# Performance work log

Hardware: AMD Instinct MI355X
Metric: run time of the kernel (lower is better)

Reference implementation:

```python
import jax, jax.numpy as jnp
import numpy as np

N_NODES = 30000
N_EDGES = 480000
IN_FEATS = 256
N_HEADS = 8
OUT_FEATS = 32
EDGE_FEATS = 64
NUM_ETYPES = 8
NEG_SLOPE = 0.2


def setup_inputs() -> dict:
    key = jax.random.key(0)
    ks = jax.random.split(key, 14)
    s = 0.05
    return {
        "feat": jax.random.normal(ks[0], (N_NODES, IN_FEATS), dtype=jnp.float32),
        "e_feat": jax.random.randint(ks[1], (N_EDGES,), 0, NUM_ETYPES, dtype=jnp.int32),
        "src": jax.random.randint(ks[2], (N_EDGES,), 0, N_NODES, dtype=jnp.int32),
        "dst": jax.random.randint(ks[3], (N_EDGES,), 0, N_NODES, dtype=jnp.int32),
        # learned params (torch nn.Linear stores weight as [out, in])
        "fc_W": jax.random.normal(ks[4], (N_HEADS * OUT_FEATS, IN_FEATS), dtype=jnp.float32) * s,
        "edge_emb": jax.random.normal(ks[5], (NUM_ETYPES, EDGE_FEATS), dtype=jnp.float32) * s,
        "w_r": jnp.ones((NUM_ETYPES, 1), dtype=jnp.float32),  # init constant 1.0
        "W1": jax.random.normal(ks[6], (EDGE_FEATS * 2, EDGE_FEATS), dtype=jnp.float32) * s,
        "b1": jnp.zeros((EDGE_FEATS * 2,), dtype=jnp.float32),
        "W2": jax.random.normal(ks[7], (EDGE_FEATS * N_HEADS, EDGE_FEATS * 2), dtype=jnp.float32) * s,
        "b2": jnp.zeros((EDGE_FEATS * N_HEADS,), dtype=jnp.float32),
        "attn_l": jax.random.normal(ks[8], (1, N_HEADS, OUT_FEATS), dtype=jnp.float32) * s,
        "attn_r": jax.random.normal(ks[9], (1, N_HEADS, OUT_FEATS), dtype=jnp.float32) * s,
        "attn_e": jax.random.normal(ks[10], (1, N_HEADS, EDGE_FEATS), dtype=jnp.float32) * s,
    }


def reference(feat, e_feat, src, dst, fc_W, edge_emb, w_r, W1, b1, W2, b2,
              attn_l, attn_r, attn_e):
    # node projection: [N, H, D]
    feat_src = (feat @ fc_W.T).reshape(N_NODES, N_HEADS, OUT_FEATS)

    # edge-type embedding -> MLP -> [E, H, edge_feats]
    e_emb = edge_emb[e_feat]                                  # [E, EF]
    h = jax.nn.relu(e_emb @ W1.T + b1)                        # [E, 2*EF]
    e_proc = (h @ W2.T + b2).reshape(-1, N_HEADS, EDGE_FEATS)  # [E, H, EF]

    ee = jnp.sum(e_proc * attn_e, axis=-1)                    # [E, H]
    el = jnp.sum(feat_src * attn_l, axis=-1)                  # [N, H]
    er = jnp.sum(feat_src * attn_r, axis=-1)                  # [N, H]

    logits = jax.nn.leaky_relu(el[src] + er[dst] + ee, NEG_SLOPE)
    logits = logits * w_r[e_feat]                             # relation weight, [E,1] bcast

    # edge_softmax: segment softmax over destination nodes
    emax = jax.ops.segment_max(logits, dst, num_segments=N_NODES)  # [N, H]
    ex = jnp.exp(logits - emax[dst])                               # [E, H]
    denom = jax.ops.segment_sum(ex, dst, num_segments=N_NODES)     # [N, H]
    a = ex / denom[dst]                                            # [E, H]

    # weighted scatter-sum aggregation: rst[v] = sum_{e: dst(e)=v} a_e * feat_src[src(e)]
    msg = feat_src[src] * a[..., None]                             # [E, H, D]
    rst = jax.ops.segment_sum(msg, dst, num_segments=N_NODES)      # [N, H, D]

    return rst, a[..., None]
```

## Files before the change

### kernel.cpp

```cpp
#include <hip/hip_runtime.h>
#include <math.h>

#define N_NODES 30000
#define N_EDGES 480000
#define IN_FEATS 256
#define N_HEADS 8
#define OUT_FEATS 32
#define EDGE_FEATS 64
#define NUM_ETYPES 8
#define NEG_SLOPE 0.2f
#define HD 256

typedef __bf16 bf16_t;
typedef bf16_t bf16x8 __attribute__((ext_vector_type(8)));
typedef float f32x4 __attribute__((ext_vector_type(4)));

__device__ __forceinline__ unsigned short f2bf(float f) {
    unsigned u = __float_as_uint(f);
    u += 0x7fffu + ((u >> 16) & 1u);
    return (unsigned short)(u >> 16);
}
__device__ __forceinline__ float bf2f(unsigned short s) {
    return __uint_as_float(((unsigned)s) << 16);
}

__device__ __forceinline__ void gload_lds16(const void* g, void* l) {
    __builtin_amdgcn_global_load_lds(
        (const __attribute__((address_space(1))) unsigned int*)g,
        (__attribute__((address_space(3))) unsigned int*)l, 16, 0, 0);
}

__global__ __launch_bounds__(1024) void ee_all(
    const float* __restrict__ edge_emb,
    const float* __restrict__ W1, const float* __restrict__ b1,
    const float* __restrict__ W2, const float* __restrict__ b2,
    const float* __restrict__ attn_e, float* __restrict__ ee_tab) {
    __shared__ float h1S[1024];
    __shared__ float MS[1024];
    const int t0 = threadIdx.x;
    {
        int t = t0 >> 7, r = t0 & 127;
        const float4* Wv = (const float4*)(W1 + (size_t)r * EDGE_FEATS);
        const float4* Ev = (const float4*)(edge_emb + (size_t)t * EDGE_FEATS);
        float s = b1[r];
        #pragma unroll
        for (int q = 0; q < 16; q++) {
            float4 w = Wv[q], e = Ev[q];
            s += w.x * e.x + w.y * e.y + w.z * e.z + w.w * e.w;
        }
        h1S[t0] = fmaxf(s, 0.f);
    }
    {
        int h = t0 >> 7, k = t0 & 127;
        float s = 0.f;
        #pragma unroll 8
        for (int f = 0; f < EDGE_FEATS; f++)
            s = fmaf(attn_e[h * EDGE_FEATS + f],
                     W2[(size_t)(h * EDGE_FEATS + f) * (2 * EDGE_FEATS) + k], s);
        MS[t0] = s;
    }
    __syncthreads();
    if (t0 < 64) {
        int t = t0 >> 3, h = t0 & 7;
        float s = 0.f;
        for (int f = 0; f < EDGE_FEATS; f++)
            s = fmaf(attn_e[h * EDGE_FEATS + f], b2[h * EDGE_FEATS + f], s);
        for (int k = 0; k < 2 * EDGE_FEATS; k++)
            s = fmaf(MS[h * 128 + k], h1S[t * 128 + k], s);
        ee_tab[t0] = s;
    }
}

__global__ void cvt_hist(const float* __restrict__ feat, const float* __restrict__ fcW,
                         const int* __restrict__ dst,
                         unsigned short* __restrict__ featb, unsigned short* __restrict__ fcWb,
                         int* __restrict__ counts) {
    const int n1 = N_NODES * IN_FEATS / 4;
    const int n2 = IN_FEATS * HD / 4;
    const int tid0 = blockIdx.x * blockDim.x + threadIdx.x;
    const int stride = gridDim.x * blockDim.x;
    for (int i = tid0; i < n1 + n2; i += stride) {
        float4 v = (i < n1) ? ((const float4*)feat)[i] : ((const float4*)fcW)[i - n1];
        ushort4 o;
        o.x = f2bf(v.x); o.y = f2bf(v.y); o.z = f2bf(v.z); o.w = f2bf(v.w);
        if (i < n1) ((ushort4*)featb)[i] = o;
        else        ((ushort4*)fcWb)[i - n1] = o;
    }
    for (int e = tid0; e < N_EDGES; e += stride)
        atomicAdd(&counts[dst[e]], 1);
}

#define GBM 128
#define GBN 64
#define GBK 64
__global__ __launch_bounds__(256) void gemm_bf16(const unsigned short* __restrict__ A,
                                                 const unsigned short* __restrict__ B,
                                                 const float* __restrict__ attn_l,
                                                 const float* __restrict__ attn_r,
                                                 unsigned short* __restrict__ Cb,
                                                 float* __restrict__ el,
                                                 float* __restrict__ er) {
    __shared__ __align__(16) unsigned char As[GBM * GBK * 2];
    __shared__ __align__(16) unsigned char Bs[GBN * GBK * 2];
    const int tid = threadIdx.x;
    const int lane = tid & 63;
    const int wid = tid >> 6;
    const int wr = wid >> 1, wc = wid & 1;
    const int row0 = blockIdx.x * GBM;
    const int col0 = blockIdx.y * GBN;

    f32x4 acc[4][2] = {};

    for (int k0 = 0; k0 < IN_FEATS; k0 += GBK) {
        __syncthreads();
        #pragma unroll
        for (int i = 0; i < 4; i++) {
            int loff = wid * 4096 + i * 1024;
            int row = (loff >> 7) + (lane >> 3);
            int c = lane & 7;
            int gr = row0 + row; if (gr > N_NODES - 1) gr = N_NODES - 1;
            int gc = k0 + ((c ^ (row & 7)) << 3);
            gload_lds16(A + (size_t)gr * IN_FEATS + gc, As + loff + lane * 16);
        }
        #pragma unroll
        for (int i = 0; i < 2; i++) {
            int loff = wid * 2048 + i * 1024;
            int row = (loff >> 7) + (lane >> 3);
            int c = lane & 7;
            int gc = k0 + ((c ^ (row & 7)) << 3);
            gload_lds16(B + (size_t)(col0 + row) * IN_FEATS + gc, Bs + loff + lane * 16);
        }
        asm volatile("s_waitcnt vmcnt(0)" ::: "memory");
        __syncthreads();
        #pragma unroll
        for (int kk = 0; kk < 2; kk++) {
            bf16x8 af[4], bfr[2];
            const int g = kk * 4 + (lane >> 4);
            #pragma unroll
            for (int fm = 0; fm < 4; fm++) {
                int row = wr * 64 + fm * 16 + (lane & 15);
                af[fm] = *(const bf16x8*)(As + row * 128 + ((g ^ (row & 7)) << 4));
            }
            #pragma unroll
            for (int fn = 0; fn < 2; fn++) {
                int row = wc * 32 + fn * 16 + (lane & 15);
                bfr[fn] = *(const bf16x8*)(Bs + row * 128 + ((g ^ (row & 7)) << 4));
            }
            #pragma unroll
            for (int fm = 0; fm < 4; fm++)
                #pragma unroll
                for (int fn = 0; fn < 2; fn++)
                    acc[fm][fn] = __builtin_amdgcn_mfma_f32_16x16x32_bf16(
                        af[fm], bfr[fn], acc[fm][fn], 0, 0, 0);
        }
    }
    #pragma unroll
    for (int fm = 0; fm < 4; fm++) {
        #pragma unroll
        for (int r = 0; r < 4; r++) {
            int row = row0 + wr * 64 + fm * 16 + (lane >> 4) * 4 + r;
            if (row < N_NODES) {
                #pragma unroll
                for (int fn = 0; fn < 2; fn++) {
                    int col = col0 + wc * 32 + fn * 16 + (lane & 15);
                    Cb[(size_t)row * HD + col] = f2bf(acc[fm][fn][r]);
                }
            }
        }
    }
    const int h = col0 / 32 + wc;
    const int d0 = lane & 15;
    const float al0 = attn_l[h * 32 + d0],  al1 = attn_l[h * 32 + d0 + 16];
    const float ar0 = attn_r[h * 32 + d0],  ar1 = attn_r[h * 32 + d0 + 16];
    #pragma unroll
    for (int fm = 0; fm < 4; fm++) {
        #pragma unroll
        for (int r = 0; r < 4; r++) {
            float sl = acc[fm][0][r] * al0 + acc[fm][1][r] * al1;
            float sr = acc[fm][0][r] * ar0 + acc[fm][1][r] * ar1;
            #pragma unroll
            for (int m = 1; m <= 8; m <<= 1) {
                sl += __shfl_xor(sl, m);
                sr += __shfl_xor(sr, m);
            }
            int row = row0 + wr * 64 + fm * 16 + (lane >> 4) * 4 + r;
            if (d0 == 0 && row < N_NODES) {
                el[row * 8 + h] = sl;
                er[row * 8 + h] = sr;
            }
        }
    }
}

__global__ __launch_bounds__(1024) void scan_kernel(const int* __restrict__ counts,
                                                    int* __restrict__ offsets,
                                                    int* __restrict__ cursor) {
    __shared__ int buf[30720];
    __shared__ int sums[1024];
    const int t = threadIdx.x;
    const int per = 30;
    for (int i = t; i < 30720; i += 1024)
        buf[i] = (i < N_NODES) ? counts[i] : 0;
    __syncthreads();
    int s = 0;
    #pragma unroll
    for (int i = 0; i < per; i++) s += buf[t * per + i];
    sums[t] = s;
    __syncthreads();
    for (int off = 1; off < 1024; off <<= 1) {
        int v = (t >= off) ? sums[t - off] : 0;
        __syncthreads();
        sums[t] += v;
        __syncthreads();
    }
    int run = sums[t] - s;
    #pragma unroll
    for (int i = 0; i < per; i++) {
        int c = buf[t * per + i];
        buf[t * per + i] = run;
        run += c;
    }
    __syncthreads();
    for (int i = t; i < N_NODES; i += 1024) {
        int v = buf[i];
        offsets[i] = v; cursor[i] = v;
    }
}

__global__ void scatter_kernel(const int* __restrict__ dst, const int* __restrict__ src,
                               const int* __restrict__ etype, int* __restrict__ cursor,
                               int2* __restrict__ sorted2) {
    int e = blockIdx.x * blockDim.x + threadIdx.x;
    if (e >= N_EDGES) return;
    int pos = atomicAdd(&cursor[dst[e]], 1);
    sorted2[pos] = make_int2(src[e] * 8 + etype[e], e);
}

__global__ __launch_bounds__(256) void node_fused(
    const int* __restrict__ offsets, const int* __restrict__ counts,
    const int2* __restrict__ sorted2,
    const float* __restrict__ el, const float* __restrict__ er,
    const float* __restrict__ ee_tab, const float* __restrict__ w_r,
    const unsigned short* __restrict__ fsb,
    float* __restrict__ rst, float* __restrict__ aOut) {
    __shared__ float eeS[64];
    __shared__ float wrS[8];
    __shared__ float lgS[4][64][8];
    __shared__ int   sS[4][8];
    if (threadIdx.x < 64) eeS[threadIdx.x] = ee_tab[threadIdx.x];
    if (threadIdx.x < 8)  wrS[threadIdx.x] = w_r[threadIdx.x];
    __syncthreads();
    const int wv = threadIdx.x >> 6, lane = threadIdx.x & 63;
    const int node = blockIdx.x * 4 + wv;
    if (node >= N_NODES) return;
    const int beg = offsets[node], cnt = counts[node];
    const int e_l = lane >> 3, h = lane & 7;
    const float er_v = er[node * 8 + h];
    const int nch = (cnt + 7) >> 3;

    float m = -1e30f;
    for (int ch = 0; ch < nch; ch++) {
        int idx = ch * 8 + e_l;
        float lg = -1e30f;
        if (idx < cnt) {
            int2 p = sorted2[beg + idx];
            int s = p.x >> 3, t = p.x & 7;
            float x = el[s * 8 + h] + er_v + eeS[t * 8 + h];
            x = (x > 0.f) ? x : NEG_SLOPE * x;
            lg = x * wrS[t];
        }
        if (idx < 64) lgS[wv][idx][h] = lg;
        m = fmaxf(m, lg);
    }
    m = fmaxf(m, __shfl_xor(m, 8));
    m = fmaxf(m, __shfl_xor(m, 16));
    m = fmaxf(m, __shfl_xor(m, 32));

    float sum = 0.f;
    for (int ch = 0; ch < nch; ch++) {
        int idx = ch * 8 + e_l;
        if (idx < cnt) {
            float lg;
            if (idx < 64) lg = lgS[wv][idx][h];
            else {
                int2 p = sorted2[beg + idx];
                int s = p.x >> 3, t = p.x & 7;
                float x = el[s * 8 + h] + er_v + eeS[t * 8 + h];
                x = (x > 0.f) ? x : NEG_SLOPE * x;
                lg = x * wrS[t];
            }
            sum += __expf(lg - m);
        }
    }
    sum += __shfl_xor(sum, 8);
    sum += __shfl_xor(sum, 16);
    sum += __shfl_xor(sum, 32);
    const float inv = 1.f / sum;

    float acc0 = 0.f, acc1 = 0.f, acc2 = 0.f, acc3 = 0.f;
    const int hq = lane >> 3;
    for (int ch = 0; ch < nch; ch++) {
        int idx = ch * 8 + e_l;
        float a = 0.f; int s = 0;
        if (idx < cnt) {
            int2 p = sorted2[beg + idx];
            s = p.x >> 3;
            float lg;
            if (idx < 64) lg = lgS[wv][idx][h];
            else {
                int t = p.x & 7;
                float x = el[s * 8 + h] + er_v + eeS[t * 8 + h];
                x = (x > 0.f) ? x : NEG_SLOPE * x;
                lg = x * wrS[t];
            }
            a = __expf(lg - m) * inv;
            aOut[(size_t)p.y * 8 + h] = a;
        }
        lgS[wv][idx & 63][h] = a;
        if (h == 0) sS[wv][e_l] = s;
        int lim = cnt - ch * 8; if (lim > 8) lim = 8;
        for (int j = 0; j < lim; j++) {
            int sj = sS[wv][j];
            float av = lgS[wv][(ch * 8 + j) & 63][hq];
            ushort4 u = *(const ushort4*)(fsb + (size_t)sj * HD + lane * 4);
            acc0 = fmaf(av, bf2f(u.x), acc0);
            acc1 = fmaf(av, bf2f(u.y), acc1);
            acc2 = fmaf(av, bf2f(u.z), acc2);
            acc3 = fmaf(av, bf2f(u.w), acc3);
        }
    }
    *(float4*)(rst + (size_t)node * HD + lane * 4) = make_float4(acc0, acc1, acc2, acc3);
}

extern "C" void kernel_launch(void* const* d_in, const int* in_sizes, int n_in,
                              void* d_out, int out_size, void* d_ws, size_t ws_size,
                              hipStream_t stream) {
    const float* feat     = (const float*)d_in[0];
    const int*   e_feat   = (const int*)  d_in[1];
    const int*   src      = (const int*)  d_in[2];
    const int*   dst      = (const int*)  d_in[3];
    const float* fc_W     = (const float*)d_in[4];
    const float* edge_emb = (const float*)d_in[5];
    const float* w_r      = (const float*)d_in[6];
    const float* W1       = (const float*)d_in[7];
    const float* b1       = (const float*)d_in[8];
    const float* W2       = (const float*)d_in[9];
    const float* b2       = (const float*)d_in[10];
    const float* attn_l   = (const float*)d_in[11];
    const float* attn_r   = (const float*)d_in[12];
    const float* attn_e   = (const float*)d_in[13];

    char* ws = (char*)d_ws;
    unsigned short* featb  = (unsigned short*)(ws + 0);
    unsigned short* fsb    = (unsigned short*)(ws + 15360000);
    float*          el     = (float*)(ws + 30720000);
    float*          er     = (float*)(ws + 31680000);
    unsigned short* fcWb   = (unsigned short*)(ws + 32640000);
    float*          ee_tab = (float*)(ws + 32771072);
    int*            counts = (int*)(ws + 32771328);
    int*            offs   = (int*)(ws + 32891328);
    int*            cursor = (int*)(ws + 33011328);
    int2*           sorted2= (int2*)(ws + 33131328);

    float* rst  = (float*)d_out;
    float* aOut = rst + (size_t)N_NODES * HD;

    hipMemsetAsync(counts, 0, 120000, stream);
    ee_all<<<1, 1024, 0, stream>>>(edge_emb, W1, b1, W2, b2, attn_e, ee_tab);
    cvt_hist<<<2048, 256, 0, stream>>>(feat, fc_W, dst, featb, fcWb, counts);
    scan_kernel<<<1, 1024, 0, stream>>>(counts, offs, cursor);
    scatter_kernel<<<(N_EDGES + 255) / 256, 256, 0, stream>>>(dst, src, e_feat, cursor, sorted2);
    gemm_bf16<<<dim3((N_NODES + GBM - 1) / GBM, HD / GBN), 256, 0, stream>>>(
        featb, fcWb, attn_l, attn_r, fsb, el, er);
    node_fused<<<(N_NODES + 3) / 4, 256, 0, stream>>>(
        offs, counts, sorted2, el, er, ee_tab, w_r, fsb, rst, aOut);
}
```

Measured before the change: 256.8 us.

## Merge edge-table and scan kernels; double-buffer GEMM with wider 128x128 tiles

```diff
diff --git a/kernel.cpp b/kernel.cpp
--- a/kernel.cpp
+++ b/kernel.cpp
@@ -28,47 +28,6 @@
     __builtin_amdgcn_global_load_lds(
         (const __attribute__((address_space(1))) unsigned int*)g,
         (__attribute__((address_space(3))) unsigned int*)l, 16, 0, 0);
-}
-
-__global__ __launch_bounds__(1024) void ee_all(
-    const float* __restrict__ edge_emb,
-    const float* __restrict__ W1, const float* __restrict__ b1,
-    const float* __restrict__ W2, const float* __restrict__ b2,
-    const float* __restrict__ attn_e, float* __restrict__ ee_tab) {
-    __shared__ float h1S[1024];
-    __shared__ float MS[1024];
-    const int t0 = threadIdx.x;
-    {
-        int t = t0 >> 7, r = t0 & 127;
-        const float4* Wv = (const float4*)(W1 + (size_t)r * EDGE_FEATS);
-        const float4* Ev = (const float4*)(edge_emb + (size_t)t * EDGE_FEATS);
-        float s = b1[r];
-        #pragma unroll
-        for (int q = 0; q < 16; q++) {
-            float4 w = Wv[q], e = Ev[q];
-            s += w.x * e.x + w.y * e.y + w.z * e.z + w.w * e.w;
-        }
-        h1S[t0] = fmaxf(s, 0.f);
-    }
-    {
-        int h = t0 >> 7, k = t0 & 127;
-        float s = 0.f;
-        #pragma unroll 8
-        for (int f = 0; f < EDGE_FEATS; f++)
-            s = fmaf(attn_e[h * EDGE_FEATS + f],
-                     W2[(size_t)(h * EDGE_FEATS + f) * (2 * EDGE_FEATS) + k], s);
-        MS[t0] = s;
-    }
-    __syncthreads();
-    if (t0 < 64) {
-        int t = t0 >> 3, h = t0 & 7;
-        float s = 0.f;
-        for (int f = 0; f < EDGE_FEATS; f++)
-            s = fmaf(attn_e[h * EDGE_FEATS + f], b2[h * EDGE_FEATS + f], s);
-        for (int k = 0; k < 2 * EDGE_FEATS; k++)
-            s = fmaf(MS[h * 128 + k], h1S[t * 128 + k], s);
-        ee_tab[t0] = s;
-    }
 }
 
 __global__ void cvt_hist(const float* __restrict__ feat, const float* __restrict__ fcW,
@@ -90,48 +49,125 @@
         atomicAdd(&counts[dst[e]], 1);
 }
 
+__global__ __launch_bounds__(1024) void ee_scan(
+    const float* __restrict__ edge_emb,
+    const float* __restrict__ W1, const float* __restrict__ b1,
+    const float* __restrict__ W2, const float* __restrict__ b2,
+    const float* __restrict__ attn_e, float* __restrict__ ee_tab,
+    const int* __restrict__ counts, int* __restrict__ offsets,
+    int* __restrict__ cursor) {
+    __shared__ float h1S[1024];
+    __shared__ float MS[1024];
+    __shared__ int   buf[30720];
+    __shared__ int   sums[1024];
+    const int t0 = threadIdx.x;
+
+    {
+        int t = t0 >> 7, r = t0 & 127;
+        const float4* Wv = (const float4*)(W1 + (size_t)r * EDGE_FEATS);
+        const float4* Ev = (const float4*)(edge_emb + (size_t)t * EDGE_FEATS);
+        float s = b1[r];
+        #pragma unroll
+        for (int q = 0; q < 16; q++) {
+            float4 w = Wv[q], e = Ev[q];
+            s += w.x * e.x + w.y * e.y + w.z * e.z + w.w * e.w;
+        }
+        h1S[t0] = fmaxf(s, 0.f);
+    }
+    {
+        int h = t0 >> 7, k = t0 & 127;
+        float s = 0.f;
+        #pragma unroll 8
+        for (int f = 0; f < EDGE_FEATS; f++)
+            s = fmaf(attn_e[h * EDGE_FEATS + f],
+                     W2[(size_t)(h * EDGE_FEATS + f) * (2 * EDGE_FEATS) + k], s);
+        MS[t0] = s;
+    }
+    __syncthreads();
+    if (t0 < 64) {
+        int t = t0 >> 3, h = t0 & 7;
+        float s = 0.f;
+        for (int f = 0; f < EDGE_FEATS; f++)
+            s = fmaf(attn_e[h * EDGE_FEATS + f], b2[h * EDGE_FEATS + f], s);
+        for (int k = 0; k < 2 * EDGE_FEATS; k++)
+            s = fmaf(MS[h * 128 + k], h1S[t * 128 + k], s);
+        ee_tab[t0] = s;
+    }
+
+    for (int i = t0; i < 30720; i += 1024)
+        buf[i] = (i < N_NODES) ? counts[i] : 0;
+    __syncthreads();
+    int s = 0;
+    #pragma unroll
+    for (int i = 0; i < 30; i++) s += buf[t0 * 30 + i];
+    sums[t0] = s;
+    __syncthreads();
+    for (int off = 1; off < 1024; off <<= 1) {
+        int v = (t0 >= off) ? sums[t0 - off] : 0;
+        __syncthreads();
+        sums[t0] += v;
+        __syncthreads();
+    }
+    int run = sums[t0] - s;
+    #pragma unroll
+    for (int i = 0; i < 30; i++) {
+        int c = buf[t0 * 30 + i];
+        buf[t0 * 30 + i] = run;
+        run += c;
+    }
+    __syncthreads();
+    for (int i = t0; i < N_NODES; i += 1024) {
+        int v = buf[i];
+        offsets[i] = v; cursor[i] = v;
+    }
+}
+
 #define GBM 128
-#define GBN 64
+#define GBN 128
 #define GBK 64
-__global__ __launch_bounds__(256) void gemm_bf16(const unsigned short* __restrict__ A,
+__global__ __launch_bounds__(512) void gemm_bf16(const unsigned short* __restrict__ A,
                                                  const unsigned short* __restrict__ B,
                                                  const float* __restrict__ attn_l,
                                                  const float* __restrict__ attn_r,
                                                  unsigned short* __restrict__ Cb,
                                                  float* __restrict__ el,
                                                  float* __restrict__ er) {
-    __shared__ __align__(16) unsigned char As[GBM * GBK * 2];
-    __shared__ __align__(16) unsigned char Bs[GBN * GBK * 2];
-    const int tid = threadIdx.x;
-    const int lane = tid & 63;
-    const int wid = tid >> 6;
-    const int wr = wid >> 1, wc = wid & 1;
+    __shared__ __align__(16) unsigned char As[2][GBM * GBK * 2];
+    __shared__ __align__(16) unsigned char Bs[2][GBN * GBK * 2];
+    const int lane = threadIdx.x & 63;
+    const int wid = threadIdx.x >> 6;
+    const int wr = wid >> 2, wc = wid & 3;
     const int row0 = blockIdx.x * GBM;
     const int col0 = blockIdx.y * GBN;
 
     f32x4 acc[4][2] = {};
 
-    for (int k0 = 0; k0 < IN_FEATS; k0 += GBK) {
-        __syncthreads();
-        #pragma unroll
-        for (int i = 0; i < 4; i++) {
-            int loff = wid * 4096 + i * 1024;
+    auto STAGE = [&](int b, int k0) {
+        #pragma unroll
+        for (int i = 0; i < 2; i++) {
+            int loff = (wid * 2 + i) * 1024;
             int row = (loff >> 7) + (lane >> 3);
             int c = lane & 7;
             int gr = row0 + row; if (gr > N_NODES - 1) gr = N_NODES - 1;
             int gc = k0 + ((c ^ (row & 7)) << 3);
-            gload_lds16(A + (size_t)gr * IN_FEATS + gc, As + loff + lane * 16);
+            gload_lds16(A + (size_t)gr * IN_FEATS + gc, As[b] + loff + lane * 16);
         }
         #pragma unroll
         for (int i = 0; i < 2; i++) {
-            int loff = wid * 2048 + i * 1024;
+            int loff = (wid * 2 + i) * 1024;
             int row = (loff >> 7) + (lane >> 3);
             int c = lane & 7;
             int gc = k0 + ((c ^ (row & 7)) << 3);
-            gload_lds16(B + (size_t)(col0 + row) * IN_FEATS + gc, Bs + loff + lane * 16);
-        }
-        asm volatile("s_waitcnt vmcnt(0)" ::: "memory");
-        __syncthreads();
+            gload_lds16(B + (size_t)(col0 + row) * IN_FEATS + gc, Bs[b] + loff + lane * 16);
+        }
+    };
+
+    STAGE(0, 0);
+    __syncthreads();
+    int cur = 0;
+    #pragma unroll
+    for (int kt = 0; kt < IN_FEATS / GBK; kt++) {
+        if (kt < IN_FEATS / GBK - 1) STAGE(cur ^ 1, (kt + 1) * GBK);
         #pragma unroll
         for (int kk = 0; kk < 2; kk++) {
             bf16x8 af[4], bfr[2];
@@ -139,12 +175,12 @@
             #pragma unroll
             for (int fm = 0; fm < 4; fm++) {
                 int row = wr * 64 + fm * 16 + (lane & 15);
-                af[fm] = *(const bf16x8*)(As + row * 128 + ((g ^ (row & 7)) << 4));
+                af[fm] = *(const bf16x8*)(As[cur] + row * 128 + ((g ^ (row & 7)) << 4));
             }
             #pragma unroll
             for (int fn = 0; fn < 2; fn++) {
                 int row = wc * 32 + fn * 16 + (lane & 15);
-                bfr[fn] = *(const bf16x8*)(Bs + row * 128 + ((g ^ (row & 7)) << 4));
+                bfr[fn] = *(const bf16x8*)(Bs[cur] + row * 128 + ((g ^ (row & 7)) << 4));
             }
             #pragma unroll
             for (int fm = 0; fm < 4; fm++)
@@ -153,6 +189,8 @@
                     acc[fm][fn] = __builtin_amdgcn_mfma_f32_16x16x32_bf16(
                         af[fm], bfr[fn], acc[fm][fn], 0, 0, 0);
         }
+        __syncthreads();
+        cur ^= 1;
     }
     #pragma unroll
     for (int fm = 0; fm < 4; fm++) {
@@ -189,41 +227,6 @@
                 er[row * 8 + h] = sr;
             }
         }
-    }
-}
-
-__global__ __launch_bounds__(1024) void scan_kernel(const int* __restrict__ counts,
-                                                    int* __restrict__ offsets,
-                                                    int* __restrict__ cursor) {
-    __shared__ int buf[30720];
-    __shared__ int sums[1024];
-    const int t = threadIdx.x;
-    const int per = 30;
-    for (int i = t; i < 30720; i += 1024)
-        buf[i] = (i < N_NODES) ? counts[i] : 0;
-    __syncthreads();
-    int s = 0;
-    #pragma unroll
-    for (int i = 0; i < per; i++) s += buf[t * per + i];
-    sums[t] = s;
-    __syncthreads();
-    for (int off = 1; off < 1024; off <<= 1) {
-        int v = (t >= off) ? sums[t - off] : 0;
-        __syncthreads();
-        sums[t] += v;
-        __syncthreads();
-    }
-    int run = sums[t] - s;
-    #pragma unroll
-    for (int i = 0; i < per; i++) {
-        int c = buf[t * per + i];
-        buf[t * per + i] = run;
-        run += c;
-    }
-    __syncthreads();
-    for (int i = t; i < N_NODES; i += 1024) {
-        int v = buf[i];
-        offsets[i] = v; cursor[i] = v;
     }
 }
 
@@ -366,11 +369,11 @@
     float* aOut = rst + (size_t)N_NODES * HD;
 
     hipMemsetAsync(counts, 0, 120000, stream);
-    ee_all<<<1, 1024, 0, stream>>>(edge_emb, W1, b1, W2, b2, attn_e, ee_tab);
     cvt_hist<<<2048, 256, 0, stream>>>(feat, fc_W, dst, featb, fcWb, counts);
-    scan_kernel<<<1, 1024, 0, stream>>>(counts, offs, cursor);
+    ee_scan<<<1, 1024, 0, stream>>>(edge_emb, W1, b1, W2, b2, attn_e, ee_tab,
+                                    counts, offs, cursor);
     scatter_kernel<<<(N_EDGES + 255) / 256, 256, 0, stream>>>(dst, src, e_feat, cursor, sorted2);
-    gemm_bf16<<<dim3((N_NODES + GBM - 1) / GBM, HD / GBN), 256, 0, stream>>>(
+    gemm_bf16<<<dim3((N_NODES + GBM - 1) / GBM, HD / GBN), 512, 0, stream>>>(
         featb, fcWb, attn_l, attn_r, fsb, el, er);
     node_fused<<<(N_NODES + 3) / 4, 256, 0, stream>>>(
         offs, counts, sorted2, el, er, ee_tab, w_r, fsb, rst, aOut);
```

Result: faster. 248.8 us (-3.1%).
